# Kernel optimization log

Measured on AMD Instinct MI355X. Metric: run time of the kernel, lower is better.

The kernel has to match this reference:

```python
import jax, jax.numpy as jnp
import numpy as np

BN_EPS = 1e-5
SG = jax.lax.stop_gradient


def _silu(z):
    return z * jax.nn.sigmoid(z)


def _binary_activation(x):
    # forward value = sign(x); backward goes through piecewise quadratic out3 (STE)
    out1 = jnp.where(x < -1, -1.0, x * x + 2 * x)
    out2 = jnp.where(x < 0, out1, -x * x + 2 * x)
    out3 = jnp.where(x < 1, out2, 1.0)
    return SG(jnp.sign(x)) - SG(out3) + out3


def _binarize_weight(w):
    # per-output-channel scaling factor * sign(w), STE through clipped weights
    sf = SG(jnp.mean(jnp.abs(w), axis=(1, 2, 3), keepdims=True))  # [O,1,1,1]
    cw = jnp.clip(w, -1.0, 1.0)
    return SG(sf * jnp.sign(w)) - SG(cw) + cw


def _conv3x3_s2(x, w, b):
    y = jax.lax.conv_general_dilated(
        x, w, window_strides=(2, 2), padding=((1, 1), (1, 1)),
        dimension_numbers=("NCHW", "OIHW", "NCHW"))
    return y + b[None, :, None, None]


def _batchnorm_train(x, gamma, beta):
    # training-mode BN: batch statistics over (N,H,W), biased variance
    mean = jnp.mean(x, axis=(0, 2, 3), keepdims=True)
    var = jnp.mean((x - mean) ** 2, axis=(0, 2, 3), keepdims=True)
    xhat = (x - mean) * jax.lax.rsqrt(var + BN_EPS)
    return xhat * gamma[None, :, None, None] + beta[None, :, None, None]


def _learnable_bias(x, emb, w, b):
    # bias = zero_module(linear)(SiLU(emb)) broadcast over H,W
    bias = _silu(emb) @ w.T + b  # [B, C]
    return x + bias[:, :, None, None]


def _avgpool2(x):
    B, C, H, W = x.shape
    return x.reshape(B, C, H // 2, 2, W // 2, 2).mean(axis=(3, 5))


def setup_inputs() -> dict:
    key = jax.random.key(0)
    ks = jax.random.split(key, 16)
    B, Cin, P, E, H, W = 32, 128, 256, 512, 64, 64
    scalor = P // Cin  # 2
    inp = {
        "x": jax.random.normal(ks[0], (B, Cin, H, W), jnp.float32),
        "emb": jax.random.normal(ks[1], (B, E), jnp.float32),
        "m1_w": jax.random.normal(ks[2], (Cin, E), jnp.float32) * 0.02,
        "m1_b": jnp.zeros((Cin,), jnp.float32),
        "conv_w": jax.random.uniform(ks[3], (scalor, Cin, Cin, 3, 3), jnp.float32, -1.0, 1.0) * 0.1,
        "conv_b": jax.random.normal(ks[4], (scalor, Cin), jnp.float32) * 0.01,
        "bn_g": jnp.ones((scalor, Cin), jnp.float32),
        "bn_b": jnp.zeros((scalor, Cin), jnp.float32),
        "m2_w": jax.random.normal(ks[5], (P, E), jnp.float32) * 0.02,
        "m2_b": jnp.zeros((P,), jnp.float32),
        "prelu_a": jnp.full((P,), 0.25, jnp.float32),
        "m3_w": jax.random.normal(ks[6], (P, E), jnp.float32) * 0.02,
        "m3_b": jnp.zeros((P,), jnp.float32),
    }
    return inp


def reference(x, emb, m1_w, m1_b, conv_w, conv_b, bn_g, bn_b,
              m2_w, m2_b, prelu_a, m3_w, m3_b):
    scalor = conv_w.shape[0]
    out = _learnable_bias(x, emb, m1_w, m1_b)
    out = _binary_activation(out)
    xp = _avgpool2(x)  # residual, [B,Cin,H/2,W/2]
    out_list = []
    for i in range(scalor):
        bw = _binarize_weight(conv_w[i])
        y = _conv3x3_s2(out, bw, conv_b[i])
        y = _batchnorm_train(y, bn_g[i], bn_b[i])
        out_list.append(y + xp)
    o = jnp.concatenate(out_list, axis=1)  # [B, planes, H/2, W/2]
    o = _learnable_bias(o, emb, m2_w, m2_b)
    a = prelu_a[None, :, None, None]
    o = jnp.where(o > 0, o, a * o)  # PReLU per channel
    o = _learnable_bias(o, emb, m3_w, m3_b)
    return o
```

## Files before the change

kernel.cpp:

```cpp
#include <hip/hip_runtime.h>
#include <cstdint>
#include <cstddef>

#define B_  32
#define CIN 128
#define P_  256
#define E_  512
#define H_  64
#define W_  64
#define HO  32
#define WO  32

__global__ void k_init(const float* __restrict__ emb, float* __restrict__ se,
                       float* __restrict__ s12) {
    int i = blockIdx.x * 256 + threadIdx.x;
    if (i < B_ * E_) {
        float e = emb[i];
        se[i] = e / (1.f + expf(-e));
    } else if (i < B_ * E_ + 2 * P_) {
        s12[i - B_ * E_] = 0.f;
    }
}

__global__ void k_bias(const float* __restrict__ se,
                       const float* __restrict__ m1_w, const float* __restrict__ m1_b,
                       const float* __restrict__ m2_w, const float* __restrict__ m2_b,
                       const float* __restrict__ m3_w, const float* __restrict__ m3_b,
                       float* __restrict__ b1, float* __restrict__ b2, float* __restrict__ b3) {
    int bid = blockIdx.x;
    int n = bid / 160, rg = bid % 160;
    int wave = threadIdx.x >> 6, lane = threadIdx.x & 63;
    int row = rg * 4 + wave;
    const float* sp = se + n * E_;
    const float* wrow; float bias; float* dst;
    if (row < CIN)            { wrow = m1_w + (size_t)row * E_;           bias = m1_b[row]; dst = b1 + n * CIN + row; }
    else if (row < CIN + P_)  { int c = row - CIN;       wrow = m2_w + (size_t)c * E_; bias = m2_b[c]; dst = b2 + n * P_ + c; }
    else                      { int c = row - CIN - P_;  wrow = m3_w + (size_t)c * E_; bias = m3_b[c]; dst = b3 + n * P_ + c; }
    float acc = 0.f;
    #pragma unroll
    for (int j = 0; j < 8; j++) {
        int k = j * 64 + lane;
        acc += sp[k] * wrow[k];
    }
    #pragma unroll
    for (int off = 32; off > 0; off >>= 1) acc += __shfl_down(acc, off);
    if (lane == 0) *dst = acc + bias;
}

__global__ void k_wprep(const float* __restrict__ conv_w,
                        float* __restrict__ sf, unsigned int* __restrict__ wbits) {
    int oc = blockIdx.x;
    int i  = threadIdx.x;
    const float* wp = conv_w + ((size_t)oc * CIN + i) * 9;
    float w[9]; float s = 0.f;
    #pragma unroll
    for (int t = 0; t < 9; t++) { w[t] = wp[t]; s += fabsf(w[t]); }
    int wave = i >> 6, lane = i & 63;
    #pragma unroll
    for (int t = 0; t < 9; t++) {
        unsigned long long m = __ballot(w[t] < 0.f);
        if (lane == 0) {
            wbits[oc * 36 + t * 4 + wave * 2 + 0] = (unsigned int)(m & 0xffffffffull);
            wbits[oc * 36 + t * 4 + wave * 2 + 1] = (unsigned int)(m >> 32);
        }
    }
    __shared__ float red[128];
    red[i] = s; __syncthreads();
    for (int st = 64; st > 0; st >>= 1) {
        if (i < st) red[i] += red[i + st];
        __syncthreads();
    }
    if (i == 0) sf[oc] = red[0] / 1152.f;
}

__global__ void k_abits(const float* __restrict__ x, const float* __restrict__ b1,
                        unsigned int* __restrict__ abits) {
    int idx = blockIdx.x * blockDim.x + threadIdx.x;
    int w = idx & 63, h = (idx >> 6) & 63, n = idx >> 12;
    const float* xpp = x + ((size_t)n * CIN) * (H_ * W_) + h * W_ + w;
    const float* bp = b1 + n * CIN;
    unsigned int words[4];
    #pragma unroll
    for (int wd = 0; wd < 4; wd++) {
        unsigned int m = 0;
        #pragma unroll
        for (int b = 0; b < 32; b++) {
            int c = wd * 32 + b;
            float v = xpp[(size_t)c * (H_ * W_)] + bp[c];
            m |= (v < 0.f ? 1u : 0u) << b;
        }
        words[wd] = m;
    }
    ((uint4*)abits)[idx] = make_uint4(words[0], words[1], words[2], words[3]);
}

__global__ void k_xp(const float* __restrict__ x, float* __restrict__ xpool) {
    int idx = blockIdx.x * blockDim.x + threadIdx.x;
    int w = idx & 31, h = (idx >> 5) & 31;
    int c = (idx >> 10) & 127, n = idx >> 17;
    const float* p = x + (((size_t)n * CIN + c) * H_ + 2 * h) * W_ + 2 * w;
    float2 a = *(const float2*)p;
    float2 b = *(const float2*)(p + W_);
    xpool[idx] = 0.25f * (a.x + a.y + b.x + b.y);
}

__global__ void __launch_bounds__(256, 4) k_conv(const unsigned int* __restrict__ abits,
                                                 const unsigned int* __restrict__ wbits,
                                                 const float* __restrict__ sf,
                                                 float* __restrict__ y) {
    __shared__ __align__(16) uint4 swb[32 * 9];
    int bid = blockIdx.x;
    int strip = bid & 3;
    int ocg   = (bid >> 2) & 7;
    int n     = bid >> 5;
    int tid = threadIdx.x;
    int oh = strip * 8 + (tid >> 5), ow = tid & 31;

    const uint4* wsrc = ((const uint4*)wbits) + (size_t)ocg * 32 * 9;
    for (int i = tid; i < 32 * 9; i += 256) swb[i] = wsrc[i];

    const uint4* asrc = ((const uint4*)abits) + ((size_t)n << 12);
    uint4 img[9];
    int vmask = 0;
    #pragma unroll
    for (int kh = 0; kh < 3; kh++) {
        #pragma unroll
        for (int kw = 0; kw < 3; kw++) {
            int t = kh * 3 + kw;
            int r = 2 * oh - 1 + kh, c = 2 * ow - 1 + kw;
            bool v = (unsigned)r < 64u && (unsigned)c < 64u;
            img[t] = v ? asrc[r * 64 + c] : make_uint4(0u, 0u, 0u, 0u);
            vmask |= (v ? 1 : 0) << t;
        }
    }
    int base128 = 128 * __popc(vmask);
    __syncthreads();

    float* yp = y + (((size_t)n * P_ + ocg * 32) << 10) + strip * 256 + tid;
    const float* sfp = sf + ocg * 32;
    #pragma unroll 2
    for (int o = 0; o < 32; o++) {
        int popsum = 0;
        #pragma unroll
        for (int t = 0; t < 9; t++) {
            uint4 a = img[t];
            uint4 w = swb[o * 9 + t];
            int p = __popc(a.x ^ w.x) + __popc(a.y ^ w.y) +
                    __popc(a.z ^ w.z) + __popc(a.w ^ w.w);
            popsum += ((vmask >> t) & 1) ? p : 0;
        }
        float val = sfp[o] * (float)(base128 - 2 * popsum);
        yp[(size_t)o << 10] = val;
    }
}

__global__ void k_stats(const float* __restrict__ y,
                        float* __restrict__ s1, float* __restrict__ s2) {
    int c = blockIdx.x >> 2, q = blockIdx.x & 3;
    int tid = threadIdx.x;
    float s = 0.f, ss = 0.f;
    for (int n = q * 8; n < q * 8 + 8; n++) {
        float4 v = ((const float4*)y)[(((size_t)n * P_ + c) << 8) + tid];
        s  += v.x + v.y + v.z + v.w;
        ss += v.x * v.x + v.y * v.y + v.z * v.z + v.w * v.w;
    }
    #pragma unroll
    for (int off = 32; off > 0; off >>= 1) {
        s += __shfl_down(s, off); ss += __shfl_down(ss, off);
    }
    __shared__ float r1[4], r2[4];
    int wave = tid >> 6, lane = tid & 63;
    if (lane == 0) { r1[wave] = s; r2[wave] = ss; }
    __syncthreads();
    if (tid == 0) {
        atomicAdd(s1 + c, r1[0] + r1[1] + r1[2] + r1[3]);
        atomicAdd(s2 + c, r2[0] + r2[1] + r2[2] + r2[3]);
    }
}

__global__ void k_epi(float* __restrict__ y, const float* __restrict__ xpool,
                      const float* __restrict__ s1, const float* __restrict__ s2,
                      const float* __restrict__ bn_g, const float* __restrict__ bn_b,
                      const float* __restrict__ b2, const float* __restrict__ b3,
                      const float* __restrict__ prelu_a) {
    int i4 = blockIdx.x * blockDim.x + threadIdx.x;
    int pix4 = i4 & 255;
    int c = (i4 >> 8) & 255;
    int n = i4 >> 16;
    float4 yv = ((const float4*)y)[i4];
    float4 xv = ((const float4*)xpool)[((n * CIN + (c & 127)) << 8) + pix4];
    const float inv = 1.f / (B_ * HO * WO);
    float m = s1[c] * inv;
    float var = fmaf(-m, m, s2[c] * inv);
    float r = rsqrtf(var + 1e-5f) * bn_g[c];
    float add0 = bn_b[c] + b2[n * P_ + c];
    float a = prelu_a[c];
    float b3v = b3[n * P_ + c];
    float o0 = (yv.x - m) * r + add0 + xv.x; o0 = (o0 > 0.f ? o0 : a * o0) + b3v;
    float o1 = (yv.y - m) * r + add0 + xv.y; o1 = (o1 > 0.f ? o1 : a * o1) + b3v;
    float o2 = (yv.z - m) * r + add0 + xv.z; o2 = (o2 > 0.f ? o2 : a * o2) + b3v;
    float o3 = (yv.w - m) * r + add0 + xv.w; o3 = (o3 > 0.f ? o3 : a * o3) + b3v;
    ((float4*)y)[i4] = make_float4(o0, o1, o2, o3);
}

extern "C" void kernel_launch(void* const* d_in, const int* in_sizes, int n_in,
                              void* d_out, int out_size, void* d_ws, size_t ws_size,
                              hipStream_t stream) {
    const float* x      = (const float*)d_in[0];
    const float* emb    = (const float*)d_in[1];
    const float* m1_w   = (const float*)d_in[2];
    const float* m1_b   = (const float*)d_in[3];
    const float* conv_w = (const float*)d_in[4];
    const float* bn_g   = (const float*)d_in[6];
    const float* bn_b   = (const float*)d_in[7];
    const float* m2_w   = (const float*)d_in[8];
    const float* m2_b   = (const float*)d_in[9];
    const float* prelu_a= (const float*)d_in[10];
    const float* m3_w   = (const float*)d_in[11];
    const float* m3_b   = (const float*)d_in[12];

    float* y = (float*)d_out;

    float* wsf = (float*)d_ws;
    float* se    = wsf;
    float* b1    = wsf + 16384;
    float* b2    = wsf + 20480;
    float* b3    = wsf + 28672;
    float* sf    = wsf + 36864;
    float* s1    = wsf + 37120;
    float* s2    = wsf + 37376;
    unsigned int* wbits = (unsigned int*)(wsf + 37632);
    unsigned int* abits = (unsigned int*)(wsf + 46848);
    float* xpool = wsf + 571136;

    k_init <<<(B_ * E_ + 2 * P_ + 255) / 256, 256, 0, stream>>>(emb, se, s1);
    k_bias <<<B_ * 160, 256, 0, stream>>>(se, m1_w, m1_b, m2_w, m2_b, m3_w, m3_b, b1, b2, b3);
    k_wprep<<<P_, 128, 0, stream>>>(conv_w, sf, wbits);
    k_abits<<<(B_ * H_ * W_) / 256, 256, 0, stream>>>(x, b1, abits);
    k_xp   <<<(B_ * CIN * HO * WO) / 256, 256, 0, stream>>>(x, xpool);
    k_conv <<<B_ * 32, 256, 0, stream>>>(abits, wbits, sf, y);
    k_stats<<<P_ * 4, 256, 0, stream>>>(y, s1, s2);
    k_epi  <<<(B_ * P_ * HO * WO) / (4 * 256), 256, 0, stream>>>(y, xpool, s1, s2,
                                                                 bn_g, bn_b, b2, b3, prelu_a);
}
```

Before: 199.5 us.

## Fuse binary conv, BN stats and epilogue into cooperative grid-synced kernel

Replaces the conv, stats and epilogue kernels with a single cooperative kernel of 256 blocks of 1024 threads. Each block keeps its 32 conv outputs per thread in registers, reduces BN sums with wave shuffles plus atomics, grid-syncs, then applies BN, residual, PReLU and biases directly. This avoids writing and rereading the intermediate conv output. SiLU is folded into the bias kernel, and the activation-bit packing and avgpool kernels are merged. The risks are a cooperative launch that needs all blocks co-resident (with a fallback path if it fails), 32-float register arrays at 1024 threads, and atomic ordering nondeterminism.

```diff
diff --git a/kernel.cpp b/kernel.cpp
--- a/kernel.cpp
+++ b/kernel.cpp
@@ -1,6 +1,9 @@
 #include <hip/hip_runtime.h>
+#include <hip/hip_cooperative_groups.h>
 #include <cstdint>
 #include <cstddef>
+
+namespace cg = cooperative_groups;
 
 #define B_  32
 #define CIN 128
@@ -11,18 +14,7 @@
 #define HO  32
 #define WO  32
 
-__global__ void k_init(const float* __restrict__ emb, float* __restrict__ se,
-                       float* __restrict__ s12) {
-    int i = blockIdx.x * 256 + threadIdx.x;
-    if (i < B_ * E_) {
-        float e = emb[i];
-        se[i] = e / (1.f + expf(-e));
-    } else if (i < B_ * E_ + 2 * P_) {
-        s12[i - B_ * E_] = 0.f;
-    }
-}
-
-__global__ void k_bias(const float* __restrict__ se,
+__global__ void k_bias(const float* __restrict__ emb,
                        const float* __restrict__ m1_w, const float* __restrict__ m1_b,
                        const float* __restrict__ m2_w, const float* __restrict__ m2_b,
                        const float* __restrict__ m3_w, const float* __restrict__ m3_b,
@@ -31,7 +23,7 @@
     int n = bid / 160, rg = bid % 160;
     int wave = threadIdx.x >> 6, lane = threadIdx.x & 63;
     int row = rg * 4 + wave;
-    const float* sp = se + n * E_;
+    const float* sp = emb + n * E_;
     const float* wrow; float bias; float* dst;
     if (row < CIN)            { wrow = m1_w + (size_t)row * E_;           bias = m1_b[row]; dst = b1 + n * CIN + row; }
     else if (row < CIN + P_)  { int c = row - CIN;       wrow = m2_w + (size_t)c * E_; bias = m2_b[c]; dst = b2 + n * P_ + c; }
@@ -40,7 +32,9 @@
     #pragma unroll
     for (int j = 0; j < 8; j++) {
         int k = j * 64 + lane;
-        acc += sp[k] * wrow[k];
+        float e = sp[k];
+        float s = e / (1.f + expf(-e));
+        acc += s * wrow[k];
     }
     #pragma unroll
     for (int off = 32; off > 0; off >>= 1) acc += __shfl_down(acc, off);
@@ -48,9 +42,11 @@
 }
 
 __global__ void k_wprep(const float* __restrict__ conv_w,
-                        float* __restrict__ sf, unsigned int* __restrict__ wbits) {
+                        float* __restrict__ sf, unsigned int* __restrict__ wbits,
+                        float* __restrict__ s1, float* __restrict__ s2) {
     int oc = blockIdx.x;
     int i  = threadIdx.x;
+    if (i == 0) { s1[oc] = 0.f; s2[oc] = 0.f; }
     const float* wp = conv_w + ((size_t)oc * CIN + i) * 9;
     float w[9]; float s = 0.f;
     #pragma unroll
@@ -73,35 +69,138 @@
     if (i == 0) sf[oc] = red[0] / 1152.f;
 }
 
-__global__ void k_abits(const float* __restrict__ x, const float* __restrict__ b1,
-                        unsigned int* __restrict__ abits) {
-    int idx = blockIdx.x * blockDim.x + threadIdx.x;
-    int w = idx & 63, h = (idx >> 6) & 63, n = idx >> 12;
-    const float* xpp = x + ((size_t)n * CIN) * (H_ * W_) + h * W_ + w;
-    const float* bp = b1 + n * CIN;
-    unsigned int words[4];
-    #pragma unroll
-    for (int wd = 0; wd < 4; wd++) {
+__global__ void k_prep(const float* __restrict__ x, const float* __restrict__ b1,
+                       unsigned int* __restrict__ abits, float* __restrict__ xpool) {
+    __shared__ float sb1[CIN];
+    int n = blockIdx.x >> 5, h2 = blockIdx.x & 31;
+    int tid = threadIdx.x;
+    for (int i = tid; i < CIN; i += 256) sb1[i] = b1[n * CIN + i];
+    __syncthreads();
+
+    int pix = tid >> 1, half = tid & 1;
+    int h = 2 * h2 + (pix >> 6), w = pix & 63;
+    const float* xp = x + ((size_t)n * CIN + half * 64) * (H_ * W_) + (size_t)h * W_ + w;
+    unsigned int wds[2];
+    #pragma unroll
+    for (int wd = 0; wd < 2; wd++) {
         unsigned int m = 0;
         #pragma unroll
         for (int b = 0; b < 32; b++) {
-            int c = wd * 32 + b;
-            float v = xpp[(size_t)c * (H_ * W_)] + bp[c];
+            float v = xp[(size_t)(wd * 32 + b) * (H_ * W_)] + sb1[half * 64 + wd * 32 + b];
             m |= (v < 0.f ? 1u : 0u) << b;
         }
-        words[wd] = m;
-    }
-    ((uint4*)abits)[idx] = make_uint4(words[0], words[1], words[2], words[3]);
-}
-
-__global__ void k_xp(const float* __restrict__ x, float* __restrict__ xpool) {
-    int idx = blockIdx.x * blockDim.x + threadIdx.x;
-    int w = idx & 31, h = (idx >> 5) & 31;
-    int c = (idx >> 10) & 127, n = idx >> 17;
-    const float* p = x + (((size_t)n * CIN + c) * H_ + 2 * h) * W_ + 2 * w;
-    float2 a = *(const float2*)p;
-    float2 b = *(const float2*)(p + W_);
-    xpool[idx] = 0.25f * (a.x + a.y + b.x + b.y);
+        wds[wd] = m;
+    }
+    ((uint2*)abits)[((size_t)n * 4096 + (size_t)h * 64 + w) * 2 + half] = make_uint2(wds[0], wds[1]);
+
+    for (int idx = tid; idx < CIN * WO; idx += 256) {
+        int c = idx >> 5, w2 = idx & 31;
+        const float* p = x + ((size_t)n * CIN + c) * (H_ * W_) + (size_t)(2 * h2) * W_ + 2 * w2;
+        float2 a = *(const float2*)p;
+        float2 b = *(const float2*)(p + W_);
+        xpool[((size_t)n * CIN + c) * (HO * WO) + h2 * WO + w2] = 0.25f * (a.x + a.y + b.x + b.y);
+    }
+}
+
+__global__ void __launch_bounds__(1024, 4) k_conv_fused(
+        const unsigned int* __restrict__ abits,
+        const unsigned int* __restrict__ wbits,
+        const float* __restrict__ sf,
+        const float* __restrict__ xpool,
+        float* __restrict__ s1, float* __restrict__ s2,
+        const float* __restrict__ bn_g, const float* __restrict__ bn_b,
+        const float* __restrict__ b2, const float* __restrict__ b3,
+        const float* __restrict__ prelu_a,
+        float* __restrict__ y) {
+    __shared__ __align__(16) uint4 swb[32 * 9];
+    __shared__ float red1[16][32], red2[16][32];
+    __shared__ float Lm[32], Lr[32], La[32], Ladd[32], Lb3[32];
+
+    int bid = blockIdx.x;
+    int ocg = bid & 7, n = bid >> 3;
+    int tid = threadIdx.x;
+    int oh = tid >> 5, ow = tid & 31;
+
+    const uint4* wsrc = ((const uint4*)wbits) + (size_t)ocg * 32 * 9;
+    for (int i = tid; i < 32 * 9; i += 1024) swb[i] = wsrc[i];
+
+    const uint4* asrc = ((const uint4*)abits) + ((size_t)n << 12);
+    uint4 img[9];
+    int vmask = 0;
+    #pragma unroll
+    for (int kh = 0; kh < 3; kh++) {
+        #pragma unroll
+        for (int kw = 0; kw < 3; kw++) {
+            int t = kh * 3 + kw;
+            int r = 2 * oh - 1 + kh, c = 2 * ow - 1 + kw;
+            bool v = (unsigned)r < 64u && (unsigned)c < 64u;
+            img[t] = v ? asrc[r * 64 + c] : make_uint4(0u, 0u, 0u, 0u);
+            vmask |= (v ? 1 : 0) << t;
+        }
+    }
+    int base128 = 128 * __popc(vmask);
+    __syncthreads();
+
+    int wave = tid >> 6, lane = tid & 63;
+    const float* sfp = sf + ocg * 32;
+    float val[32];
+    #pragma unroll
+    for (int o = 0; o < 32; o++) {
+        int popsum = 0;
+        #pragma unroll
+        for (int t = 0; t < 9; t++) {
+            uint4 a = img[t];
+            uint4 w = swb[o * 9 + t];
+            int p = __popc(a.x ^ w.x) + __popc(a.y ^ w.y) +
+                    __popc(a.z ^ w.z) + __popc(a.w ^ w.w);
+            popsum += ((vmask >> t) & 1) ? p : 0;
+        }
+        float v = sfp[o] * (float)(base128 - 2 * popsum);
+        val[o] = v;
+        float vs = v, v2 = v * v;
+        #pragma unroll
+        for (int off = 32; off > 0; off >>= 1) {
+            vs += __shfl_down(vs, off); v2 += __shfl_down(v2, off);
+        }
+        if (lane == 0) { red1[wave][o] = vs; red2[wave][o] = v2; }
+    }
+    __syncthreads();
+    if (tid < 32) {
+        float a = 0.f;
+        #pragma unroll
+        for (int wv = 0; wv < 16; wv++) a += red1[wv][tid];
+        atomicAdd(s1 + ocg * 32 + tid, a);
+    } else if (tid < 64) {
+        int o = tid - 32;
+        float a = 0.f;
+        #pragma unroll
+        for (int wv = 0; wv < 16; wv++) a += red2[wv][o];
+        atomicAdd(s2 + ocg * 32 + o, a);
+    }
+
+    cg::this_grid().sync();
+
+    if (tid < 32) {
+        int c = ocg * 32 + tid;
+        const float inv = 1.f / (B_ * HO * WO);
+        float m = s1[c] * inv;
+        float var = fmaf(-m, m, s2[c] * inv);
+        float r = rsqrtf(var + 1e-5f) * bn_g[c];
+        Lm[tid] = m; Lr[tid] = r;
+        La[tid] = prelu_a[c];
+        Ladd[tid] = bn_b[c] + b2[n * P_ + c];
+        Lb3[tid] = b3[n * P_ + c];
+    }
+    __syncthreads();
+
+    const float* xpb = xpool + (((size_t)n * CIN + (ocg & 3) * 32) << 10) + tid;
+    float* yp = y + (((size_t)n * P_ + ocg * 32) << 10) + tid;
+    #pragma unroll
+    for (int o = 0; o < 32; o++) {
+        float vv = (val[o] - Lm[o]) * Lr[o] + Ladd[o] + xpb[(size_t)o << 10];
+        vv = vv > 0.f ? vv : La[o] * vv;
+        yp[(size_t)o << 10] = vv + Lb3[o];
+    }
 }
 
 __global__ void __launch_bounds__(256, 4) k_conv(const unsigned int* __restrict__ abits,
@@ -110,18 +209,13 @@
                                                  float* __restrict__ y) {
     __shared__ __align__(16) uint4 swb[32 * 9];
     int bid = blockIdx.x;
-    int strip = bid & 3;
-    int ocg   = (bid >> 2) & 7;
-    int n     = bid >> 5;
+    int strip = bid & 3, ocg = (bid >> 2) & 7, n = bid >> 5;
     int tid = threadIdx.x;
     int oh = strip * 8 + (tid >> 5), ow = tid & 31;
-
     const uint4* wsrc = ((const uint4*)wbits) + (size_t)ocg * 32 * 9;
     for (int i = tid; i < 32 * 9; i += 256) swb[i] = wsrc[i];
-
     const uint4* asrc = ((const uint4*)abits) + ((size_t)n << 12);
-    uint4 img[9];
-    int vmask = 0;
+    uint4 img[9]; int vmask = 0;
     #pragma unroll
     for (int kh = 0; kh < 3; kh++) {
         #pragma unroll
@@ -135,7 +229,6 @@
     }
     int base128 = 128 * __popc(vmask);
     __syncthreads();
-
     float* yp = y + (((size_t)n * P_ + ocg * 32) << 10) + strip * 256 + tid;
     const float* sfp = sf + ocg * 32;
     #pragma unroll 2
@@ -149,8 +242,7 @@
                     __popc(a.z ^ w.z) + __popc(a.w ^ w.w);
             popsum += ((vmask >> t) & 1) ? p : 0;
         }
-        float val = sfp[o] * (float)(base128 - 2 * popsum);
-        yp[(size_t)o << 10] = val;
+        yp[(size_t)o << 10] = sfp[o] * (float)(base128 - 2 * popsum);
     }
 }
 
@@ -222,24 +314,29 @@
     float* y = (float*)d_out;
 
     float* wsf = (float*)d_ws;
-    float* se    = wsf;
-    float* b1    = wsf + 16384;
-    float* b2    = wsf + 20480;
-    float* b3    = wsf + 28672;
-    float* sf    = wsf + 36864;
-    float* s1    = wsf + 37120;
-    float* s2    = wsf + 37376;
-    unsigned int* wbits = (unsigned int*)(wsf + 37632);
-    unsigned int* abits = (unsigned int*)(wsf + 46848);
-    float* xpool = wsf + 571136;
-
-    k_init <<<(B_ * E_ + 2 * P_ + 255) / 256, 256, 0, stream>>>(emb, se, s1);
-    k_bias <<<B_ * 160, 256, 0, stream>>>(se, m1_w, m1_b, m2_w, m2_b, m3_w, m3_b, b1, b2, b3);
-    k_wprep<<<P_, 128, 0, stream>>>(conv_w, sf, wbits);
-    k_abits<<<(B_ * H_ * W_) / 256, 256, 0, stream>>>(x, b1, abits);
-    k_xp   <<<(B_ * CIN * HO * WO) / 256, 256, 0, stream>>>(x, xpool);
-    k_conv <<<B_ * 32, 256, 0, stream>>>(abits, wbits, sf, y);
-    k_stats<<<P_ * 4, 256, 0, stream>>>(y, s1, s2);
-    k_epi  <<<(B_ * P_ * HO * WO) / (4 * 256), 256, 0, stream>>>(y, xpool, s1, s2,
-                                                                 bn_g, bn_b, b2, b3, prelu_a);
-}
+    float* b1    = wsf;
+    float* b2    = wsf + 4096;
+    float* b3    = wsf + 12288;
+    float* sf    = wsf + 20480;
+    float* s1    = wsf + 20736;
+    float* s2    = wsf + 20992;
+    unsigned int* wbits = (unsigned int*)(wsf + 21248);
+    unsigned int* abits = (unsigned int*)(wsf + 30464);
+    float* xpool = wsf + 554752;
+
+    k_bias <<<B_ * 160, 256, 0, stream>>>(emb, m1_w, m1_b, m2_w, m2_b, m3_w, m3_b, b1, b2, b3);
+    k_wprep<<<P_, 128, 0, stream>>>(conv_w, sf, wbits, s1, s2);
+    k_prep <<<B_ * 32, 256, 0, stream>>>(x, b1, abits, xpool);
+
+    void* cargs[] = { (void*)&abits, (void*)&wbits, (void*)&sf, (void*)&xpool,
+                      (void*)&s1, (void*)&s2, (void*)&bn_g, (void*)&bn_b,
+                      (void*)&b2, (void*)&b3, (void*)&prelu_a, (void*)&y };
+    hipError_t err = hipLaunchCooperativeKernel((const void*)k_conv_fused, dim3(P_), dim3(1024),
+                                                cargs, 0, stream);
+    if (err != hipSuccess) {
+        k_conv <<<B_ * 32, 256, 0, stream>>>(abits, wbits, sf, y);
+        k_stats<<<P_ * 4, 256, 0, stream>>>(y, s1, s2);
+        k_epi  <<<(B_ * P_ * HO * WO) / (4 * 256), 256, 0, stream>>>(y, xpool, s1, s2,
+                                                                     bn_g, bn_b, b2, b3, prelu_a);
+    }
+}
```

Measured after the change: 241.8 us. 1.21x slower.
